# Optimization experiments

Measured on AMD Instinct MI355X. Metric: run time of the kernel, lower is better.

The kernel has to match this reference:

```python
import jax, jax.numpy as jnp
import numpy as np

N = 4096
C = 64
B = 4
DIST_THRESHOLD = 0.5
ALPHA = 0.01
NEG_INF = -1e15


def setup_inputs() -> dict:
    key = jax.random.key(0)
    k1, k2, k3, k4, k5 = jax.random.split(key, 5)
    x = jax.random.normal(k1, (B, N, C), dtype=jnp.float32)
    dist_mat = jax.random.uniform(k2, (N, N), dtype=jnp.float32)
    proj_w = jax.random.normal(k3, (N, C, C), dtype=jnp.float32) / np.sqrt(C)
    proj_b = jax.random.normal(k4, (N, C), dtype=jnp.float32) * 0.01
    a_w = jax.random.normal(k5, (N, 2 * C), dtype=jnp.float32) / np.sqrt(2 * C)
    return {"x": x, "dist_mat": dist_mat, "proj_w": proj_w, "proj_b": proj_b, "a_w": a_w}


def reference(x, dist_mat, proj_w, proj_b, a_w):
    # Adjacency: (0 < dist < threshold), diagonal forced to 1.
    adj = (dist_mat > 0) & (dist_mat < DIST_THRESHOLD)
    adj = adj | jnp.eye(N, dtype=bool)

    # Per-node projection (GraphDense): h[b,n,:] = x[b,n,:] @ proj_w[n] + proj_b[n]
    h = jnp.einsum('bnc,nco->bno', x, proj_w) + proj_b  # [B, N, C]

    # Attention score: a[j] . concat(h_i, h_j) without materializing [B,N,N,2C].
    a_src, a_dst = a_w[:, :C], a_w[:, C:]               # each [N, C]
    s = jnp.einsum('bic,jc->bij', h, a_src) + jnp.einsum('bjc,jc->bj', h, a_dst)[:, None, :]
    s = jnp.where(s >= 0, s, ALPHA * s)                 # LeakyReLU
    s = jnp.where(adj[None, :, :], s, NEG_INF)          # mask non-edges
    att = jax.nn.softmax(s, axis=-1)                    # [B, N, N]

    # Weighted aggregation over neighbors.
    y = jnp.einsum('bij,bjc->bic', att, h)              # [B, N, C]
    return y
```

## Files before the change

kernel.cpp:

```cpp
#include <hip/hip_runtime.h>

#define N 4096
#define C 64
#define B 4

typedef __attribute__((ext_vector_type(8))) short short8;
typedef __attribute__((ext_vector_type(4))) short s16x4;
typedef __attribute__((ext_vector_type(4))) float f32x4;
typedef unsigned long long u64;

#define MFMA16(a, b, c) __builtin_amdgcn_mfma_f32_16x16x32_bf16(a, b, c, 0, 0, 0)

__device__ __forceinline__ short f2bf(float f) {
    unsigned u = __builtin_bit_cast(unsigned, f);
    u += 0x7fffu + ((u >> 16) & 1u);
    return (short)(u >> 16);
}

__global__ __launch_bounds__(256) void mask_kernel(const float* __restrict__ dist,
                                                   u64* __restrict__ msk) {
    const int wave = threadIdx.x >> 6, lane = threadIdx.x & 63;
    const int i = blockIdx.x * 4 + wave;
    const float* row = dist + (size_t)i * N;
#pragma unroll 8
    for (int jb = 0; jb < N / 64; jb++) {
        float d = row[jb * 64 + lane];
        u64 m = __ballot(d > 0.f && d < 0.5f);
        int dj = i - jb * 64;
        if (dj >= 0 && dj < 64) m |= (1ull << dj);
        if (lane == 0) msk[(size_t)i * (N / 64) + jb] = m;
    }
}

__global__ __launch_bounds__(256) void proj_kernel(
    const float* __restrict__ x,
    const float* __restrict__ proj_w,
    const float* __restrict__ proj_b,
    const float* __restrict__ a_w,
    short* __restrict__ h_bf,
    short* __restrict__ a_srcb,
    float* __restrict__ e2)
{
    __shared__ float lds_w[4][64 * 64];
    __shared__ float lds_x[4][B][C];

    const int tid = threadIdx.x;
    const int wave = tid >> 6;
    const int lane = tid & 63;
    const int n = blockIdx.x * 4 + wave;
    const float* Wn = proj_w + (size_t)n * C * C;

    float4 wbuf[16];
#pragma unroll
    for (int it = 0; it < 16; it++)
        wbuf[it] = *(const float4*)(Wn + it * 256 + lane * 4);
#pragma unroll
    for (int b = 0; b < B; b++)
        lds_x[wave][b][lane] = x[((size_t)b * N + n) * C + lane];
#pragma unroll
    for (int it = 0; it < 16; it++)
        *(float4*)&lds_w[wave][it * 256 + lane * 4] = wbuf[it];

    const int o = lane;
    float acc[B];
    float pb = proj_b[(size_t)n * C + o];
#pragma unroll
    for (int b = 0; b < B; b++) acc[b] = pb;

#pragma unroll 4
    for (int c4 = 0; c4 < C; c4 += 4) {
        f32x4 xq[B];
#pragma unroll
        for (int b = 0; b < B; b++) xq[b] = *(const f32x4*)&lds_x[wave][b][c4];
#pragma unroll
        for (int k = 0; k < 4; k++) {
            float w = lds_w[wave][(c4 + k) * C + o];
#pragma unroll
            for (int b = 0; b < B; b++) acc[b] = fmaf(xq[b][k], w, acc[b]);
        }
    }

    float adst = a_w[(size_t)n * (2 * C) + C + o];
    a_srcb[(size_t)n * C + o] = f2bf(a_w[(size_t)n * (2 * C) + o]);
#pragma unroll
    for (int b = 0; b < B; b++) {
        h_bf[((size_t)b * N + n) * C + o] = f2bf(acc[b]);
        float prod = acc[b] * adst;
#pragma unroll
        for (int off = 32; off; off >>= 1) prod += __shfl_xor(prod, off, 64);
        if (lane == 0) e2[b * N + n] = prod;
    }
}

__global__ __launch_bounds__(256) void transpose_kernel(const short* __restrict__ h_bf,
                                                        short* __restrict__ hT_bf) {
    __shared__ short tile[64][72];
    const int t = threadIdx.x;
    const int b = blockIdx.y;
    const int n0 = blockIdx.x * 64;
    {
        int r = t >> 2, cs = (t & 3) * 16;
        const short* src = h_bf + ((size_t)b * N + n0 + r) * C + cs;
#pragma unroll
        for (int q = 0; q < 4; q++)
            *(s16x4*)&tile[r][cs + q * 4] = *(const s16x4*)(src + q * 4);
    }
    __syncthreads();
    {
        int c = t >> 2, ns = (t & 3) * 16;
        short v[16];
#pragma unroll
        for (int k = 0; k < 16; k++) v[k] = tile[ns + k][c];
        short* dst = hT_bf + (size_t)b * C * N + (size_t)c * N + n0 + ns;
        *(short8*)dst = *(short8*)&v[0];
        *(short8*)(dst + 8) = *(short8*)&v[8];
    }
}

__global__ __launch_bounds__(256) void attn_kernel(
    const u64* __restrict__ msk,
    const short* __restrict__ h_bf,
    const short* __restrict__ hT_bf,
    const short* __restrict__ a_srcb,
    const float* __restrict__ e2,
    float* __restrict__ part_y,
    float* __restrict__ part_m,
    float* __restrict__ part_l,
    int JS, int mode)
{
    __shared__ short lds_p[4][16 * 72];
    __shared__ float lds_e2[4][512];
    __shared__ float lds_bc[4][64];

    const int tid = threadIdx.x;
    const int wave = tid >> 6;
    const int lane = tid & 63;
    const int cl = lane & 15;
    const int rg = lane >> 4;
    const int b = wave;
    const int i0 = blockIdx.x * 32;
    const int jbeg = blockIdx.y * JS;
    const bool e2lds = (JS <= 512);

    if (e2lds) {
        for (int q = lane * 4; q < JS; q += 256)
            *(f32x4*)&lds_e2[wave][q] = *(const f32x4*)(e2 + (size_t)b * N + jbeg + q);
    }

    short8 bfr[2][2];
#pragma unroll
    for (int u = 0; u < 2; u++) {
        const short* hrow = h_bf + ((size_t)b * N + i0 + u * 16 + cl) * C;
        bfr[u][0] = *(const short8*)(hrow + rg * 8);
        bfr[u][1] = *(const short8*)(hrow + 32 + rg * 8);
    }

    const u64* mr[2] = {msk + (size_t)(i0 + cl) * (N / 64),
                        msk + (size_t)(i0 + 16 + cl) * (N / 64)};

    f32x4 yacc[2][4];
#pragma unroll
    for (int u = 0; u < 2; u++)
#pragma unroll
        for (int t = 0; t < 4; t++) { f32x4 z = {0.f, 0.f, 0.f, 0.f}; yacc[u][t] = z; }
    float m_s[2] = {-1e30f, -1e30f};
    float l_s[2] = {0.f, 0.f};

    for (int j0 = jbeg; j0 < jbeg + JS; j0 += 64) {
        short8 a0[4], a1[4];
#pragma unroll
        for (int t = 0; t < 4; t++) {
            const short* arow = a_srcb + (size_t)(j0 + t * 16 + cl) * C + rg * 8;
            a0[t] = *(const short8*)(arow);
            a1[t] = *(const short8*)(arow + 32);
        }
        f32x4 e2q[4];
#pragma unroll
        for (int t = 0; t < 4; t++) {
            if (e2lds) e2q[t] = *(const f32x4*)&lds_e2[wave][j0 - jbeg + t * 16 + rg * 4];
            else       e2q[t] = *(const f32x4*)(e2 + (size_t)b * N + j0 + t * 16 + rg * 4);
        }
        u64 mbits[2] = {mr[0][j0 >> 6], mr[1][j0 >> 6]};

        short8 pa[2][2];
#pragma unroll
        for (int u = 0; u < 2; u++) {
            f32x4 st[4];
#pragma unroll
            for (int t = 0; t < 4; t++) {
                f32x4 z = {0.f, 0.f, 0.f, 0.f};
                z = MFMA16(a0[t], bfr[u][0], z);
                z = MFMA16(a1[t], bfr[u][1], z);
                st[t] = z;
            }

            unsigned wlo = (unsigned)mbits[u], whi = (unsigned)(mbits[u] >> 32);
            float mx = -1e30f;
#pragma unroll
            for (int t = 0; t < 4; t++) {
                unsigned w = (t < 2) ? wlo : whi;
                unsigned sh = (t & 1) * 16 + rg * 4;
#pragma unroll
                for (int r = 0; r < 4; r++) {
                    float sv = st[t][r] + e2q[t][r];
                    sv = (sv >= 0.f) ? sv : 0.01f * sv;
                    sv = ((w >> (sh + r)) & 1u) ? sv : -1e15f;
                    st[t][r] = sv;
                    mx = fmaxf(mx, sv);
                }
            }

            mx = fmaxf(mx, __shfl_xor(mx, 16, 64));
            mx = fmaxf(mx, __shfl_xor(mx, 32, 64));
            float mnew = fmaxf(m_s[u], mx);
            float alpha = __expf(m_s[u] - mnew);
            m_s[u] = mnew;
            float ps = 0.f;
#pragma unroll
            for (int t = 0; t < 4; t++)
#pragma unroll
                for (int r = 0; r < 4; r++) {
                    float pv = __expf(st[t][r] - mnew);
                    st[t][r] = pv;
                    ps += pv;
                }
            ps += __shfl_xor(ps, 16, 64);
            ps += __shfl_xor(ps, 32, 64);
            l_s[u] = l_s[u] * alpha + ps;

            if (lane < 16) lds_bc[wave][u * 16 + lane] = alpha;
            f32x4 a4 = *(const f32x4*)&lds_bc[wave][u * 16 + rg * 4];
#pragma unroll
            for (int t = 0; t < 4; t++)
#pragma unroll
                for (int r = 0; r < 4; r++) yacc[u][t][r] *= a4[r];

            short* lp = lds_p[wave];
#pragma unroll
            for (int t = 0; t < 4; t++) {
                s16x4 pk;
#pragma unroll
                for (int r = 0; r < 4; r++) pk[r] = f2bf(st[t][r]);
                *(s16x4*)(lp + cl * 72 + t * 16 + rg * 4) = pk;
            }
            pa[u][0] = *(const short8*)(lp + cl * 72 + rg * 8);
            pa[u][1] = *(const short8*)(lp + cl * 72 + 32 + rg * 8);
        }

#pragma unroll
        for (int t = 0; t < 4; t++) {
            const short* hc = hT_bf + (size_t)b * C * N + (size_t)(t * 16 + cl) * N + j0 + rg * 8;
            short8 h0 = *(const short8*)(hc);
            short8 h1 = *(const short8*)(hc + 32);
            yacc[0][t] = MFMA16(pa[0][0], h0, yacc[0][t]);
            yacc[0][t] = MFMA16(pa[0][1], h1, yacc[0][t]);
            yacc[1][t] = MFMA16(pa[1][0], h0, yacc[1][t]);
            yacc[1][t] = MFMA16(pa[1][1], h1, yacc[1][t]);
        }
    }

#pragma unroll
    for (int u = 0; u < 2; u++)
        if (lane < 16) lds_bc[wave][32 + u * 16 + lane] = l_s[u];

    if (mode) {
#pragma unroll
        for (int u = 0; u < 2; u++) {
            f32x4 l4 = *(const f32x4*)&lds_bc[wave][32 + u * 16 + rg * 4];
#pragma unroll
            for (int t = 0; t < 4; t++)
#pragma unroll
                for (int r = 0; r < 4; r++)
                    part_y[((size_t)b * N + i0 + u * 16 + rg * 4 + r) * C + t * 16 + cl] =
                        yacc[u][t][r] / l4[r];
        }
    } else {
        size_t sb = (size_t)(blockIdx.y * B + b) * N;
#pragma unroll
        for (int u = 0; u < 2; u++) {
#pragma unroll
            for (int t = 0; t < 4; t++)
#pragma unroll
                for (int r = 0; r < 4; r++)
                    part_y[(sb + i0 + u * 16 + rg * 4 + r) * C + t * 16 + cl] = yacc[u][t][r];
            if (lane < 16) {
                part_m[sb + i0 + u * 16 + lane] = m_s[u];
                part_l[sb + i0 + u * 16 + lane] = l_s[u];
            }
        }
    }
}

__global__ __launch_bounds__(256) void combine_kernel(
    const float* __restrict__ part_y, const float* __restrict__ part_m,
    const float* __restrict__ part_l, float* __restrict__ out, int S)
{
    int g = blockIdx.x * 256 + threadIdx.x;
    int c = g & 63;
    int row = (g >> 6) & (N - 1);
    int b = g >> 18;
    int bn = b * N + row;
    float m = -1e30f;
    for (int s = 0; s < S; s++) m = fmaxf(m, part_m[s * (B * N) + bn]);
    float l = 0.f, y = 0.f;
    for (int s = 0; s < S; s++) {
        float w = __expf(part_m[s * (B * N) + bn] - m);
        l += part_l[s * (B * N) + bn] * w;
        y += part_y[((size_t)s * B * N + bn) * C + c] * w;
    }
    out[g] = y / l;
}

extern "C" void kernel_launch(void* const* d_in, const int* in_sizes, int n_in,
                              void* d_out, int out_size, void* d_ws, size_t ws_size,
                              hipStream_t stream) {
    const float* x      = (const float*)d_in[0];
    const float* dist   = (const float*)d_in[1];
    const float* proj_w = (const float*)d_in[2];
    const float* proj_b = (const float*)d_in[3];
    const float* a_w    = (const float*)d_in[4];
    float* out = (float*)d_out;

    char* ws = (char*)d_ws;
    short* h_bf   = (short*)(ws);
    short* hT_bf  = (short*)(ws + (2u << 20));
    short* a_srcb = (short*)(ws + (4u << 20));
    float* e2     = (float*)(ws + (4u << 20) + (512u << 10));
    u64*   msk    = (u64*)  (ws + (5u << 20));
    float* part_m = (float*)(ws + (7u << 20));
    float* part_l = (float*)(ws + (7u << 20) + (512u << 10));
    float* part_y = (float*)(ws + (8u << 20));

    proj_kernel<<<N / 4, 256, 0, stream>>>(x, proj_w, proj_b, a_w, h_bf, a_srcb, e2);
    transpose_kernel<<<dim3(N / 64, B), 256, 0, stream>>>(h_bf, hT_bf);
    mask_kernel<<<N / 4, 256, 0, stream>>>(dist, msk);

    int S = 8;
    while (S > 1 && (8u << 20) + (size_t)S * B * N * C * 4 > ws_size) S >>= 1;
    bool direct = ((8u << 20) + (size_t)B * N * C * 4 > ws_size);

    if (direct) {
        attn_kernel<<<dim3(N / 32, 1), 256, 0, stream>>>(
            msk, h_bf, hT_bf, a_srcb, e2, out, part_m, part_l, N, 1);
    } else {
        attn_kernel<<<dim3(N / 32, S), 256, 0, stream>>>(
            msk, h_bf, hT_bf, a_srcb, e2, part_y, part_m, part_l, N / S, 0);
        combine_kernel<<<(B * N * C) / 256, 256, 0, stream>>>(part_y, part_m, part_l, out, S);
    }
}
```

Baseline: 280.7 us.

## Fuse mask into projection kernel, use exp2 softmax, fold e2 into MFMA accumulator

Merges the adjacency-mask kernel into the projection kernel as extra blocks, removing one launch and letting the two independent workloads run concurrently. Pre-scales the attention weights by log2(e) so the softmax uses exp2f; this stays exact because LeakyReLU is positively homogeneous. The e2 term is now the initial MFMA accumulator instead of a separate add, and the LDS broadcasts of alpha and l are replaced with wave shuffles. The j-axis split is raised from 8 to 16 with the workspace layout adjusted, which adds parallelism in exchange for more combine traffic.

```diff
diff --git a/kernel.cpp b/kernel.cpp
--- a/kernel.cpp
+++ b/kernel.cpp
@@ -3,6 +3,7 @@
 #define N 4096
 #define C 64
 #define B 4
+#define LOG2E 1.44269504088896340736f
 
 typedef __attribute__((ext_vector_type(8))) short short8;
 typedef __attribute__((ext_vector_type(4))) short s16x4;
@@ -16,30 +17,22 @@
     u += 0x7fffu + ((u >> 16) & 1u);
     return (short)(u >> 16);
 }
-
-__global__ __launch_bounds__(256) void mask_kernel(const float* __restrict__ dist,
-                                                   u64* __restrict__ msk) {
-    const int wave = threadIdx.x >> 6, lane = threadIdx.x & 63;
-    const int i = blockIdx.x * 4 + wave;
-    const float* row = dist + (size_t)i * N;
-#pragma unroll 8
-    for (int jb = 0; jb < N / 64; jb++) {
-        float d = row[jb * 64 + lane];
-        u64 m = __ballot(d > 0.f && d < 0.5f);
-        int dj = i - jb * 64;
-        if (dj >= 0 && dj < 64) m |= (1ull << dj);
-        if (lane == 0) msk[(size_t)i * (N / 64) + jb] = m;
-    }
-}
-
-__global__ __launch_bounds__(256) void proj_kernel(
+__device__ __forceinline__ unsigned pk2bf(float a, float b) {
+    unsigned lo = (unsigned)(unsigned short)f2bf(a);
+    unsigned hi = (unsigned)(unsigned short)f2bf(b);
+    return lo | (hi << 16);
+}
+
+__global__ __launch_bounds__(256) void proj_mask_kernel(
     const float* __restrict__ x,
     const float* __restrict__ proj_w,
     const float* __restrict__ proj_b,
     const float* __restrict__ a_w,
+    const float* __restrict__ dist,
     short* __restrict__ h_bf,
     short* __restrict__ a_srcb,
-    float* __restrict__ e2)
+    float* __restrict__ e2,
+    u64* __restrict__ msk)
 {
     __shared__ float lds_w[4][64 * 64];
     __shared__ float lds_x[4][B][C];
@@ -47,6 +40,21 @@
     const int tid = threadIdx.x;
     const int wave = tid >> 6;
     const int lane = tid & 63;
+
+    if (blockIdx.x >= N / 4) {
+        const int i = (blockIdx.x - N / 4) * 4 + wave;
+        const float* row = dist + (size_t)i * N;
+#pragma unroll 8
+        for (int jb = 0; jb < N / 64; jb++) {
+            float d = row[jb * 64 + lane];
+            u64 m = __ballot(d > 0.f && d < 0.5f);
+            int dj = i - jb * 64;
+            if (dj >= 0 && dj < 64) m |= (1ull << dj);
+            if (lane == 0) msk[(size_t)i * (N / 64) + jb] = m;
+        }
+        return;
+    }
+
     const int n = blockIdx.x * 4 + wave;
     const float* Wn = proj_w + (size_t)n * C * C;
 
@@ -80,8 +88,8 @@
         }
     }
 
-    float adst = a_w[(size_t)n * (2 * C) + C + o];
-    a_srcb[(size_t)n * C + o] = f2bf(a_w[(size_t)n * (2 * C) + o]);
+    float adst = a_w[(size_t)n * (2 * C) + C + o] * LOG2E;
+    a_srcb[(size_t)n * C + o] = f2bf(a_w[(size_t)n * (2 * C) + o] * LOG2E);
 #pragma unroll
     for (int b = 0; b < B; b++) {
         h_bf[((size_t)b * N + n) * C + o] = f2bf(acc[b]);
@@ -130,7 +138,6 @@
 {
     __shared__ short lds_p[4][16 * 72];
     __shared__ float lds_e2[4][512];
-    __shared__ float lds_bc[4][64];
 
     const int tid = threadIdx.x;
     const int wave = tid >> 6;
@@ -188,8 +195,7 @@
             f32x4 st[4];
 #pragma unroll
             for (int t = 0; t < 4; t++) {
-                f32x4 z = {0.f, 0.f, 0.f, 0.f};
-                z = MFMA16(a0[t], bfr[u][0], z);
+                f32x4 z = MFMA16(a0[t], bfr[u][0], e2q[t]);
                 z = MFMA16(a1[t], bfr[u][1], z);
                 st[t] = z;
             }
@@ -202,7 +208,7 @@
                 unsigned sh = (t & 1) * 16 + rg * 4;
 #pragma unroll
                 for (int r = 0; r < 4; r++) {
-                    float sv = st[t][r] + e2q[t][r];
+                    float sv = st[t][r];
                     sv = (sv >= 0.f) ? sv : 0.01f * sv;
                     sv = ((w >> (sh + r)) & 1u) ? sv : -1e15f;
                     st[t][r] = sv;
@@ -213,14 +219,14 @@
             mx = fmaxf(mx, __shfl_xor(mx, 16, 64));
             mx = fmaxf(mx, __shfl_xor(mx, 32, 64));
             float mnew = fmaxf(m_s[u], mx);
-            float alpha = __expf(m_s[u] - mnew);
+            float alpha = exp2f(m_s[u] - mnew);
             m_s[u] = mnew;
             float ps = 0.f;
 #pragma unroll
             for (int t = 0; t < 4; t++)
 #pragma unroll
                 for (int r = 0; r < 4; r++) {
-                    float pv = __expf(st[t][r] - mnew);
+                    float pv = exp2f(st[t][r] - mnew);
                     st[t][r] = pv;
                     ps += pv;
                 }
@@ -228,8 +234,9 @@
             ps += __shfl_xor(ps, 32, 64);
             l_s[u] = l_s[u] * alpha + ps;
 
-            if (lane < 16) lds_bc[wave][u * 16 + lane] = alpha;
-            f32x4 a4 = *(const f32x4*)&lds_bc[wave][u * 16 + rg * 4];
+            float a4[4];
+#pragma unroll
+            for (int r = 0; r < 4; r++) a4[r] = __shfl(alpha, rg * 4 + r, 64);
 #pragma unroll
             for (int t = 0; t < 4; t++)
 #pragma unroll
@@ -238,10 +245,8 @@
             short* lp = lds_p[wave];
 #pragma unroll
             for (int t = 0; t < 4; t++) {
-                s16x4 pk;
-#pragma unroll
-                for (int r = 0; r < 4; r++) pk[r] = f2bf(st[t][r]);
-                *(s16x4*)(lp + cl * 72 + t * 16 + rg * 4) = pk;
+                uint2 pk = {pk2bf(st[t][0], st[t][1]), pk2bf(st[t][2], st[t][3])};
+                *(uint2*)(lp + cl * 72 + t * 16 + rg * 4) = pk;
             }
             pa[u][0] = *(const short8*)(lp + cl * 72 + rg * 8);
             pa[u][1] = *(const short8*)(lp + cl * 72 + 32 + rg * 8);
@@ -259,14 +264,12 @@
         }
     }
 
-#pragma unroll
-    for (int u = 0; u < 2; u++)
-        if (lane < 16) lds_bc[wave][32 + u * 16 + lane] = l_s[u];
-
     if (mode) {
 #pragma unroll
         for (int u = 0; u < 2; u++) {
-            f32x4 l4 = *(const f32x4*)&lds_bc[wave][32 + u * 16 + rg * 4];
+            float l4[4];
+#pragma unroll
+            for (int r = 0; r < 4; r++) l4[r] = __shfl(l_s[u], rg * 4 + r, 64);
 #pragma unroll
             for (int t = 0; t < 4; t++)
 #pragma unroll
@@ -304,7 +307,7 @@
     for (int s = 0; s < S; s++) m = fmaxf(m, part_m[s * (B * N) + bn]);
     float l = 0.f, y = 0.f;
     for (int s = 0; s < S; s++) {
-        float w = __expf(part_m[s * (B * N) + bn] - m);
+        float w = exp2f(part_m[s * (B * N) + bn] - m);
         l += part_l[s * (B * N) + bn] * w;
         y += part_y[((size_t)s * B * N + bn) * C + c] * w;
     }
@@ -328,16 +331,16 @@
     float* e2     = (float*)(ws + (4u << 20) + (512u << 10));
     u64*   msk    = (u64*)  (ws + (5u << 20));
     float* part_m = (float*)(ws + (7u << 20));
-    float* part_l = (float*)(ws + (7u << 20) + (512u << 10));
-    float* part_y = (float*)(ws + (8u << 20));
-
-    proj_kernel<<<N / 4, 256, 0, stream>>>(x, proj_w, proj_b, a_w, h_bf, a_srcb, e2);
+    float* part_l = (float*)(ws + (7u << 20) + (1u << 20));
+    float* part_y = (float*)(ws + (9u << 20));
+
+    proj_mask_kernel<<<N / 2, 256, 0, stream>>>(x, proj_w, proj_b, a_w, dist,
+                                                h_bf, a_srcb, e2, msk);
     transpose_kernel<<<dim3(N / 64, B), 256, 0, stream>>>(h_bf, hT_bf);
-    mask_kernel<<<N / 4, 256, 0, stream>>>(dist, msk);
-
-    int S = 8;
-    while (S > 1 && (8u << 20) + (size_t)S * B * N * C * 4 > ws_size) S >>= 1;
-    bool direct = ((8u << 20) + (size_t)B * N * C * 4 > ws_size);
+
+    int S = 16;
+    while (S > 1 && (9u << 20) + (size_t)S * B * N * C * 4 > ws_size) S >>= 1;
+    bool direct = ((9u << 20) + (size_t)B * N * C * 4 > ws_size);
 
     if (direct) {
         attn_kernel<<<dim3(N / 32, 1), 256, 0, stream>>>(
```

Result: slower. 320.6 us (+14.2%).
